# Optimization experiments

Measured on AMD Instinct MI355X. Metric: run time of the kernel, lower is better.

The kernel has to match this reference:

```python
import jax, jax.numpy as jnp
import numpy as np

ATT = 32      # att_size per spatial dim (pooled grid is 32x32, N=1024)
HEADS = 8

def _pool_sum(x, out):
    # adaptive max + adaptive avg pool (exact uniform windows since W%out==0)
    B, C, W, H = x.shape
    kw, kh = W // out, H // out
    r = x.reshape(B, C, out, kw, out, kh)
    return r.max(axis=(3, 5)) + r.mean(axis=(3, 5))

def _lerp_axis(x, out_len, axis):
    in_len = x.shape[axis]
    pos = jnp.arange(out_len, dtype=x.dtype) * ((in_len - 1) / (out_len - 1))
    i0 = jnp.floor(pos).astype(jnp.int32)
    i1 = jnp.minimum(i0 + 1, in_len - 1)
    t = pos - i0.astype(x.dtype)
    shp = [1] * x.ndim
    shp[axis] = out_len
    t = t.reshape(shp)
    return jnp.take(x, i0, axis=axis) * (1 - t) + jnp.take(x, i1, axis=axis) * t

def _upsample_bilinear_ac(x, out_h, out_w):
    # bilinear, align_corners=True (separable)
    return _lerp_axis(_lerp_axis(x, out_h, 2), out_w, 3)

def setup_inputs() -> dict:
    key = jax.random.key(0)
    k1, k2, k3, k4 = jax.random.split(key, 4)
    B, C, W, H = 8, 256, 128, 128
    input1 = jax.random.normal(k1, (B, C, W, H), dtype=jnp.float32)
    input2 = jax.random.normal(k2, (B, C // 2, W, H), dtype=jnp.float32)
    # 1x1 conv: out=C, in=C//2 (kaiming-ish scale)
    conv_w = jax.random.normal(k3, (C, C // 2), dtype=jnp.float32) * (1.0 / np.sqrt(C // 2))
    conv_b = jax.random.normal(k4, (C,), dtype=jnp.float32) * 0.01
    return {"input1": input1, "input2": input2, "conv_w": conv_w, "conv_b": conv_b}

def reference(input1, input2, conv_w, conv_b):
    B, C, W, H = input1.shape
    # channel projection (1x1 conv) since input2 has C//2 channels
    x2 = jnp.einsum('bihw,oi->bohw', input2, conv_w) + conv_b[None, :, None, None]
    p1 = _pool_sum(input1, ATT)   # [B,C,32,32]
    p2 = _pool_sum(x2, ATT)
    N = ATT * ATT
    q = p1.reshape(B, C, N).transpose(2, 0, 1)  # [N,B,C]
    k = p2.reshape(B, C, N).transpose(2, 0, 1)
    v = k
    scale = 1.0 / np.sqrt(C // HEADS)
    w = jnp.einsum('nbc,nec->nbe', q, k)        # [N,B,B]
    w = jax.nn.softmax(w * scale, axis=-1)
    a = jnp.einsum('nbe,nec->nbc', w, v)        # [N,B,C]
    attn = a.transpose(1, 2, 0).reshape(B, C, ATT, ATT)
    up = _upsample_bilinear_ac(attn, W, H)
    return jax.nn.sigmoid(up)
```

## Files before the change

### kernel.cpp

```cpp
#include <hip/hip_runtime.h>
#include <math.h>

namespace {

constexpr int Bn = 8, Cn = 256, CIN = 128, Wd = 128, Hd = 128, ATTn = 32, Nn = ATTn * ATTn;

typedef __attribute__((ext_vector_type(8))) short short8;
typedef __attribute__((ext_vector_type(4))) float f32x4;

__device__ inline unsigned short bf16_rne(float f) {
    unsigned int u = __float_as_uint(f);
    unsigned int r = (u + 0x7FFFu + ((u >> 16) & 1u)) >> 16;
    return (unsigned short)r;
}

__device__ inline int fsw(int px) { return (px ^ (px >> 3)) & 7; }

__global__ __launch_bounds__(512, 4) void front_kernel(const float* __restrict__ in1,
                                                       const float* __restrict__ in2,
                                                       const float* __restrict__ cw,
                                                       const float* __restrict__ cb,
                                                       float* __restrict__ p1t,
                                                       float* __restrict__ p2t) {
    __shared__ __align__(16) unsigned char smem[33792];

    const int t = threadIdx.x;
    const int bid = blockIdx.x;
    const int w = t >> 6;
    const int l = t & 63;

    if (bid < 256) {
        const int b = bid >> 5, oy = bid & 31;
        float* tile = reinterpret_cast<float*>(smem) + w * 1056;
        const int x4 = l & 31, dyp = l >> 5;
        const float* base = in1 + ((size_t)(b * Cn + w * 32) * Wd + oy * 4 + dyp) * Hd + x4 * 4;
#pragma unroll 4
        for (int ch = 0; ch < 32; ++ch) {
            const float* p = base + (size_t)ch * Wd * Hd;
            f32x4 v0 = *reinterpret_cast<const f32x4*>(p);
            f32x4 v1 = *reinterpret_cast<const f32x4*>(p + 2 * Hd);
            float mx = fmaxf(fmaxf(fmaxf(v0[0], v0[1]), fmaxf(v0[2], v0[3])),
                             fmaxf(fmaxf(v1[0], v1[1]), fmaxf(v1[2], v1[3])));
            float sm = ((v0[0] + v0[1]) + (v0[2] + v0[3])) +
                       ((v1[0] + v1[1]) + (v1[2] + v1[3]));
            mx = fmaxf(mx, __shfl_xor(mx, 32));
            sm += __shfl_xor(sm, 32);
            if (l < 32) tile[x4 * 33 + ch] = mx + sm * (1.f / 16.f);
        }
        const int cl = l & 31, oxp = l >> 5;
#pragma unroll
        for (int it = 0; it < 16; ++it) {
            const int ox = it * 2 + oxp;
            const float v = tile[ox * 33 + cl];
            p1t[((size_t)b * Nn + oy * 32 + ox) * Cn + w * 32 + cl] = v;
        }
        return;
    }

    const int bid2 = bid - 256;
    const int b = bid2 >> 7;
    const int r = bid2 & 127;
    const int oy = r >> 2, xq = r & 3;

    f32x4 ra[2][4];
    int x4v[2], rowv[2], k4v[2];
#pragma unroll
    for (int h = 0; h < 2; ++h) {
        const int i = t + h * 512;
        x4v[h] = i & 7; rowv[h] = (i >> 3) & 3; k4v[h] = i >> 5;
        const float* p = in2 + ((size_t)(b * CIN + k4v[h] * 4) * Wd + oy * 4 + rowv[h]) * Hd
                         + xq * 32 + x4v[h] * 4;
#pragma unroll
        for (int kk2 = 0; kk2 < 4; ++kk2)
            ra[h][kk2] = *reinterpret_cast<const f32x4*>(p + (size_t)kk2 * Wd * Hd);
    }

    const int n_lo = l & 15;
    const int khi = l >> 4;
    short8 bfrag[2][4];
#pragma unroll
    for (int f = 0; f < 2; ++f) {
        const int n = w * 32 + f * 16 + n_lo;
#pragma unroll
        for (int kk = 0; kk < 4; ++kk) {
            const float* wp = cw + n * CIN + kk * 32 + khi * 8;
            f32x4 va = *reinterpret_cast<const f32x4*>(wp);
            f32x4 vb = *reinterpret_cast<const f32x4*>(wp + 4);
            short8 s;
            s[0] = (short)bf16_rne(va[0]); s[1] = (short)bf16_rne(va[1]);
            s[2] = (short)bf16_rne(va[2]); s[3] = (short)bf16_rne(va[3]);
            s[4] = (short)bf16_rne(vb[0]); s[5] = (short)bf16_rne(vb[1]);
            s[6] = (short)bf16_rne(vb[2]); s[7] = (short)bf16_rne(vb[3]);
            bfrag[f][kk] = s;
        }
    }
    const float bias2_0 = 2.f * cb[w * 32 + n_lo];
    const float bias2_1 = 2.f * cb[w * 32 + 16 + n_lo];

#pragma unroll
    for (int h = 0; h < 2; ++h) {
#pragma unroll
        for (int j = 0; j < 4; ++j) {
            const int px = x4v[h] * 16 + rowv[h] * 4 + j;
            uint2 u;
            u.x = (unsigned int)bf16_rne(ra[h][0][j]) | ((unsigned int)bf16_rne(ra[h][1][j]) << 16);
            u.y = (unsigned int)bf16_rne(ra[h][2][j]) | ((unsigned int)bf16_rne(ra[h][3][j]) << 16);
            const int off = px * 256 + ((k4v[h] * 8) ^ (fsw(px) << 4));
            *reinterpret_cast<uint2*>(smem + off) = u;
        }
    }
    __syncthreads();

#pragma unroll
    for (int cl = 0; cl < 8; ++cl) {
        f32x4 acc0 = {0.f, 0.f, 0.f, 0.f};
        f32x4 acc1 = {0.f, 0.f, 0.f, 0.f};
        const int px = cl * 16 + n_lo;
        const int sw = fsw(px) << 4;
#pragma unroll
        for (int kk = 0; kk < 4; ++kk) {
            short8 a = *reinterpret_cast<const short8*>(
                smem + px * 256 + ((kk * 64 + khi * 16) ^ sw));
            acc0 = __builtin_amdgcn_mfma_f32_16x16x32_bf16(a, bfrag[0][kk], acc0, 0, 0, 0);
            acc1 = __builtin_amdgcn_mfma_f32_16x16x32_bf16(a, bfrag[1][kk], acc1, 0, 0, 0);
        }
        float mx0 = fmaxf(fmaxf(acc0[0], acc0[1]), fmaxf(acc0[2], acc0[3]));
        float sm0 = (acc0[0] + acc0[1]) + (acc0[2] + acc0[3]);
        float mx1 = fmaxf(fmaxf(acc1[0], acc1[1]), fmaxf(acc1[2], acc1[3]));
        float sm1 = (acc1[0] + acc1[1]) + (acc1[2] + acc1[3]);
        mx0 = fmaxf(mx0, __shfl_xor(mx0, 16)); sm0 += __shfl_xor(sm0, 16);
        mx0 = fmaxf(mx0, __shfl_xor(mx0, 32)); sm0 += __shfl_xor(sm0, 32);
        mx1 = fmaxf(mx1, __shfl_xor(mx1, 16)); sm1 += __shfl_xor(sm1, 16);
        mx1 = fmaxf(mx1, __shfl_xor(mx1, 32)); sm1 += __shfl_xor(sm1, 32);
        if (l < 16) {
            const int cell = oy * 32 + xq * 8 + cl;
            float* dst = p2t + ((size_t)b * Nn + cell) * Cn + w * 32 + n_lo;
            dst[0]  = mx0 + sm0 * (1.f / 16.f) + bias2_0;
            dst[16] = mx1 + sm1 * (1.f / 16.f) + bias2_1;
        }
    }
}

__global__ __launch_bounds__(256) void attn_kernel(const float* __restrict__ p1t,
                                                   const float* __restrict__ p2t,
                                                   float* __restrict__ att) {
    __shared__ float q[Bn][260];
    __shared__ float kk[Bn][260];
    __shared__ float wsm[Bn][8];
    const int n = blockIdx.x, t = threadIdx.x;

#pragma unroll
    for (int i = 0; i < 2; ++i) {
        const int f = t + i * 256;
        const int bb = f >> 6, cq = f & 63;
        const size_t off = ((size_t)bb * Nn + n) * Cn + cq * 4;
        *reinterpret_cast<float4*>(&q[bb][cq * 4])  = *reinterpret_cast<const float4*>(p1t + off);
        *reinterpret_cast<float4*>(&kk[bb][cq * 4]) = *reinterpret_cast<const float4*>(p2t + off);
    }
    __syncthreads();

    {
        const int chunk = t & 3, pair = t >> 2;
        const int e = pair & 7, bb = pair >> 3;
        float s = 0.f;
#pragma unroll
        for (int i = 0; i < 64; ++i)
            s = fmaf(q[bb][i * 4 + chunk], kk[e][i * 4 + chunk], s);
        s += __shfl_xor(s, 1);
        s += __shfl_xor(s, 2);
        s *= 0.17677669529663687f;
        float m = fmaxf(s, __shfl_xor(s, 4));
        m = fmaxf(m, __shfl_xor(m, 8));
        m = fmaxf(m, __shfl_xor(m, 16));
        float p = __expf(s - m);
        float d = p + __shfl_xor(p, 4);
        d += __shfl_xor(d, 8);
        d += __shfl_xor(d, 16);
        if (chunk == 0) wsm[bb][e] = p / d;
    }
    __syncthreads();

    float kv[8];
#pragma unroll
    for (int e = 0; e < 8; ++e) kv[e] = kk[e][t];
#pragma unroll
    for (int bb = 0; bb < 8; ++bb) {
        float s = 0.f;
#pragma unroll
        for (int e = 0; e < 8; ++e) s = fmaf(wsm[bb][e], kv[e], s);
        att[((size_t)bb * Cn + t) * Nn + n] = s;
    }
}

__global__ __launch_bounds__(256) void upsample_kernel(const float* __restrict__ att,
                                                       float* __restrict__ out) {
    __shared__ float tile[ATTn * ATTn];
    int bc = blockIdx.x, t = threadIdx.x;
    reinterpret_cast<float4*>(tile)[t] =
        reinterpret_cast<const float4*>(att + (size_t)bc * Nn)[t];
    __syncthreads();

    int tx = t & 31, ty = t >> 5;
    int xi0[4], xi1[4];
    float xt[4];
#pragma unroll
    for (int j = 0; j < 4; ++j) {
        int x = tx * 4 + j;
        float pos = (float)x * (31.f / 127.f);
        int i0 = (int)pos;
        xi0[j] = i0;
        xi1[j] = min(i0 + 1, 31);
        xt[j] = pos - (float)i0;
    }

    for (int r = 0; r < 16; ++r) {
        int y = ty + r * 8;
        float posy = (float)y * (31.f / 127.f);
        int y0 = (int)posy;
        int y1 = min(y0 + 1, 31);
        float ft = posy - (float)y0;
        float o_[4];
#pragma unroll
        for (int j = 0; j < 4; ++j) {
            float v00 = tile[y0 * 32 + xi0[j]];
            float v01 = tile[y0 * 32 + xi1[j]];
            float v10 = tile[y1 * 32 + xi0[j]];
            float v11 = tile[y1 * 32 + xi1[j]];
            float top = v00 * (1.f - ft) + v10 * ft;
            float bot = v01 * (1.f - ft) + v11 * ft;
            float val = top * (1.f - xt[j]) + bot * xt[j];
            o_[j] = 1.f / (1.f + __expf(-val));
        }
        *reinterpret_cast<float4*>(out + ((size_t)bc * Wd + y) * Hd + tx * 4) =
            make_float4(o_[0], o_[1], o_[2], o_[3]);
    }
}

}

extern "C" void kernel_launch(void* const* d_in, const int* in_sizes, int n_in,
                              void* d_out, int out_size, void* d_ws, size_t ws_size,
                              hipStream_t stream) {
    const float* input1 = (const float*)d_in[0];
    const float* input2 = (const float*)d_in[1];
    const float* conv_w = (const float*)d_in[2];
    const float* conv_b = (const float*)d_in[3];
    float* out = (float*)d_out;

    float* p1t = (float*)d_ws;
    float* p2t = p1t + (size_t)Bn * Cn * Nn;
    float* att = p2t + (size_t)Bn * Cn * Nn;

    front_kernel<<<dim3(1280), dim3(512), 0, stream>>>(input1, input2, conv_w, conv_b, p1t, p2t);
    attn_kernel<<<dim3(Nn), dim3(256), 0, stream>>>(p1t, p2t, att);
    upsample_kernel<<<dim3(Bn * Cn), dim3(256), 0, stream>>>(att, out);
}
```

Before: 110.8 us.

## Split input1 pooling into finer blocks and interleave with conv blocks

The input1 pooling branch is split from 256 large blocks into 2048 smaller blocks, each covering one output row and a 32-channel group. These are interleaved 2:1 with the conv/pool blocks so both kinds of work are spread evenly across CUs. The change also rearranges per-thread loads to 8 contiguous floats, adds shuffle reductions, and uses float2 stores through a shared tile after a barrier. It is meant to fix load imbalance and tail effects from the few heavy pooling blocks, at the cost of more blocks and an extra sync.

```diff
diff --git a/kernel.cpp b/kernel.cpp
--- a/kernel.cpp
+++ b/kernel.cpp
@@ -28,36 +28,49 @@
     const int bid = blockIdx.x;
     const int w = t >> 6;
     const int l = t & 63;
-
-    if (bid < 256) {
-        const int b = bid >> 5, oy = bid & 31;
-        float* tile = reinterpret_cast<float*>(smem) + w * 1056;
-        const int x4 = l & 31, dyp = l >> 5;
-        const float* base = in1 + ((size_t)(b * Cn + w * 32) * Wd + oy * 4 + dyp) * Hd + x4 * 4;
-#pragma unroll 4
-        for (int ch = 0; ch < 32; ++ch) {
-            const float* p = base + (size_t)ch * Wd * Hd;
-            f32x4 v0 = *reinterpret_cast<const f32x4*>(p);
-            f32x4 v1 = *reinterpret_cast<const f32x4*>(p + 2 * Hd);
-            float mx = fmaxf(fmaxf(fmaxf(v0[0], v0[1]), fmaxf(v0[2], v0[3])),
-                             fmaxf(fmaxf(v1[0], v1[1]), fmaxf(v1[2], v1[3])));
-            float sm = ((v0[0] + v0[1]) + (v0[2] + v0[3])) +
-                       ((v1[0] + v1[1]) + (v1[2] + v1[3]));
-            mx = fmaxf(mx, __shfl_xor(mx, 32));
-            sm += __shfl_xor(sm, 32);
-            if (l < 32) tile[x4 * 33 + ch] = mx + sm * (1.f / 16.f);
-        }
-        const int cl = l & 31, oxp = l >> 5;
-#pragma unroll
-        for (int it = 0; it < 16; ++it) {
-            const int ox = it * 2 + oxp;
-            const float v = tile[ox * 33 + cl];
-            p1t[((size_t)b * Nn + oy * 32 + ox) * Cn + w * 32 + cl] = v;
-        }
+    const int g3 = bid / 3;
+    const int r3 = bid - g3 * 3;
+
+    if (r3 != 2) {
+        const int p = g3 * 2 + r3;
+        const int b = p >> 8;
+        const int rem = p & 255;
+        const int oy = rem >> 3, cg = rem & 7;
+        float* tile = reinterpret_cast<float*>(smem);
+
+        const int dy = l >> 4, xp = l & 15;
+        const float* base0 = in1 + (((size_t)(b * Cn + cg * 32 + w * 4) * Wd) + oy * 4 + dy) * Hd
+                             + xp * 8;
+#pragma unroll
+        for (int c4 = 0; c4 < 4; ++c4) {
+            const float* q = base0 + (size_t)c4 * Wd * Hd;
+            f32x4 v0 = *reinterpret_cast<const f32x4*>(q);
+            f32x4 v1 = *reinterpret_cast<const f32x4*>(q + 4);
+            float mx0 = fmaxf(fmaxf(v0[0], v0[1]), fmaxf(v0[2], v0[3]));
+            float sm0 = (v0[0] + v0[1]) + (v0[2] + v0[3]);
+            float mx1 = fmaxf(fmaxf(v1[0], v1[1]), fmaxf(v1[2], v1[3]));
+            float sm1 = (v1[0] + v1[1]) + (v1[2] + v1[3]);
+            mx0 = fmaxf(mx0, __shfl_xor(mx0, 16)); sm0 += __shfl_xor(sm0, 16);
+            mx0 = fmaxf(mx0, __shfl_xor(mx0, 32)); sm0 += __shfl_xor(sm0, 32);
+            mx1 = fmaxf(mx1, __shfl_xor(mx1, 16)); sm1 += __shfl_xor(sm1, 16);
+            mx1 = fmaxf(mx1, __shfl_xor(mx1, 32)); sm1 += __shfl_xor(sm1, 32);
+            if (l < 16) {
+                const int wc = w * 4 + c4;
+                tile[(2 * xp) * 33 + wc]     = mx0 + sm0 * (1.f / 16.f);
+                tile[(2 * xp + 1) * 33 + wc] = mx1 + sm1 * (1.f / 16.f);
+            }
+        }
+        __syncthreads();
+        const int ox = t >> 4, cp = t & 15;
+        float2 o;
+        o.x = tile[ox * 33 + cp * 2];
+        o.y = tile[ox * 33 + cp * 2 + 1];
+        *reinterpret_cast<float2*>(
+            p1t + ((size_t)b * Nn + oy * 32 + ox) * Cn + cg * 32 + cp * 2) = o;
         return;
     }
 
-    const int bid2 = bid - 256;
+    const int bid2 = g3;
     const int b = bid2 >> 7;
     const int r = bid2 & 127;
     const int oy = r >> 2, xq = r & 3;
@@ -251,7 +264,7 @@
     float* p2t = p1t + (size_t)Bn * Cn * Nn;
     float* att = p2t + (size_t)Bn * Cn * Nn;
 
-    front_kernel<<<dim3(1280), dim3(512), 0, stream>>>(input1, input2, conv_w, conv_b, p1t, p2t);
+    front_kernel<<<dim3(3072), dim3(512), 0, stream>>>(input1, input2, conv_w, conv_b, p1t, p2t);
     attn_kernel<<<dim3(Nn), dim3(256), 0, stream>>>(p1t, p2t, att);
     upsample_kernel<<<dim3(Bn * Cn), dim3(256), 0, stream>>>(att, out);
 }
```

New measurement: 112.4 us. About the same (+1.5%).

## Split front kernel into separate pool1 and conv-pool kernels with finer work units

Applied to the files above, without the earlier changes.

The combined front kernel is split in two. One kernel does the max+avg pooling of input1, and the other does the 1x1 conv plus pooling of input2. The new pool1 kernel gives each wave 8 channels of one pooled row instead of 32, uses a small padded LDS tile, and writes the transposed result with 16-byte vector stores. This aims to spread the input1 pooling over many more waves and improve store coalescing, at the cost of an extra kernel launch and losing the overlap between the two heterogeneous block types.

```diff
diff --git a/kernel.cpp b/kernel.cpp
--- a/kernel.cpp
+++ b/kernel.cpp
@@ -16,48 +16,57 @@
 
 __device__ inline int fsw(int px) { return (px ^ (px >> 3)) & 7; }
 
-__global__ __launch_bounds__(512, 4) void front_kernel(const float* __restrict__ in1,
-                                                       const float* __restrict__ in2,
-                                                       const float* __restrict__ cw,
-                                                       const float* __restrict__ cb,
-                                                       float* __restrict__ p1t,
-                                                       float* __restrict__ p2t) {
-    __shared__ __align__(16) unsigned char smem[33792];
+__global__ __launch_bounds__(256, 4) void pool1_kernel(const float* __restrict__ in1,
+                                                       float* __restrict__ p1t) {
+    __shared__ float tile[4][32 * 9];
+    const int t = threadIdx.x, w = t >> 6, l = t & 63;
+    const int gw = blockIdx.x * 4 + w;
+    const int ox = l & 31, half = l >> 5;
+
+#pragma unroll
+    for (int u = 0; u < 2; ++u) {
+        const int unit = gw + u * 4096;
+        const int b = unit >> 10;
+        const int rem = unit & 1023;
+        const int oy = rem >> 5, cg = rem & 31;
+        const float* base = in1 + (((size_t)(b * Cn + cg * 8) * Wd) + oy * 4 + 2 * half) * Hd
+                            + ox * 4;
+        float res[8];
+#pragma unroll
+        for (int c = 0; c < 8; ++c) {
+            const float* p = base + (size_t)c * Wd * Hd;
+            f32x4 a  = *reinterpret_cast<const f32x4*>(p);
+            f32x4 bv = *reinterpret_cast<const f32x4*>(p + Hd);
+            float m = fmaxf(fmaxf(fmaxf(a[0], a[1]), fmaxf(a[2], a[3])),
+                            fmaxf(fmaxf(bv[0], bv[1]), fmaxf(bv[2], bv[3])));
+            float s = ((a[0] + a[1]) + (a[2] + a[3])) + ((bv[0] + bv[1]) + (bv[2] + bv[3]));
+            m = fmaxf(m, __shfl_xor(m, 32));
+            s += __shfl_xor(s, 32);
+            res[c] = m + s * (1.f / 16.f);
+        }
+        if (l < 32) {
+#pragma unroll
+            for (int c = 0; c < 8; ++c) tile[w][ox * 9 + c] = res[c];
+        }
+        const int ox2 = l >> 1, hf = l & 1;
+        f32x4 o;
+#pragma unroll
+        for (int j = 0; j < 4; ++j) o[j] = tile[w][ox2 * 9 + hf * 4 + j];
+        *reinterpret_cast<f32x4*>(
+            p1t + ((size_t)b * Nn + oy * 32 + ox2) * Cn + cg * 8 + hf * 4) = o;
+    }
+}
+
+__global__ __launch_bounds__(512, 4) void convpool_kernel(const float* __restrict__ in2,
+                                                          const float* __restrict__ cw,
+                                                          const float* __restrict__ cb,
+                                                          float* __restrict__ p2t) {
+    __shared__ __align__(16) unsigned char smem[32768];
 
     const int t = threadIdx.x;
-    const int bid = blockIdx.x;
     const int w = t >> 6;
     const int l = t & 63;
-
-    if (bid < 256) {
-        const int b = bid >> 5, oy = bid & 31;
-        float* tile = reinterpret_cast<float*>(smem) + w * 1056;
-        const int x4 = l & 31, dyp = l >> 5;
-        const float* base = in1 + ((size_t)(b * Cn + w * 32) * Wd + oy * 4 + dyp) * Hd + x4 * 4;
-#pragma unroll 4
-        for (int ch = 0; ch < 32; ++ch) {
-            const float* p = base + (size_t)ch * Wd * Hd;
-            f32x4 v0 = *reinterpret_cast<const f32x4*>(p);
-            f32x4 v1 = *reinterpret_cast<const f32x4*>(p + 2 * Hd);
-            float mx = fmaxf(fmaxf(fmaxf(v0[0], v0[1]), fmaxf(v0[2], v0[3])),
-                             fmaxf(fmaxf(v1[0], v1[1]), fmaxf(v1[2], v1[3])));
-            float sm = ((v0[0] + v0[1]) + (v0[2] + v0[3])) +
-                       ((v1[0] + v1[1]) + (v1[2] + v1[3]));
-            mx = fmaxf(mx, __shfl_xor(mx, 32));
-            sm += __shfl_xor(sm, 32);
-            if (l < 32) tile[x4 * 33 + ch] = mx + sm * (1.f / 16.f);
-        }
-        const int cl = l & 31, oxp = l >> 5;
-#pragma unroll
-        for (int it = 0; it < 16; ++it) {
-            const int ox = it * 2 + oxp;
-            const float v = tile[ox * 33 + cl];
-            p1t[((size_t)b * Nn + oy * 32 + ox) * Cn + w * 32 + cl] = v;
-        }
-        return;
-    }
-
-    const int bid2 = bid - 256;
+    const int bid2 = blockIdx.x;
     const int b = bid2 >> 7;
     const int r = bid2 & 127;
     const int oy = r >> 2, xq = r & 3;
@@ -251,7 +260,8 @@
     float* p2t = p1t + (size_t)Bn * Cn * Nn;
     float* att = p2t + (size_t)Bn * Cn * Nn;
 
-    front_kernel<<<dim3(1280), dim3(512), 0, stream>>>(input1, input2, conv_w, conv_b, p1t, p2t);
+    pool1_kernel<<<dim3(1024), dim3(256), 0, stream>>>(input1, p1t);
+    convpool_kernel<<<dim3(1024), dim3(512), 0, stream>>>(input2, conv_w, conv_b, p2t);
     attn_kernel<<<dim3(Nn), dim3(256), 0, stream>>>(p1t, p2t, att);
     upsample_kernel<<<dim3(Bn * Cn), dim3(256), 0, stream>>>(att, out);
 }
```

Result: slower. 114.1 us (+3.0%).

## Split fused pool/conv front kernel into separate pooling and conv-pool kernels

Applied to the files above, without the earlier changes.

The pooling of input1 moves out of the combined front kernel into its own kernel. The new kernel launches 8192 small 256-thread blocks, each handling 8 channels by one output row. The conv+pool part becomes its own kernel with slightly less shared memory. This targets the load imbalance of the old combined grid, where 256 heavy pooling blocks each looped over 32 channels alongside the conv blocks. The cost is an extra kernel launch and the loss of any overlap between the two front phases within one launch.

```diff
diff --git a/kernel.cpp b/kernel.cpp
--- a/kernel.cpp
+++ b/kernel.cpp
@@ -16,48 +16,44 @@
 
 __device__ inline int fsw(int px) { return (px ^ (px >> 3)) & 7; }
 
-__global__ __launch_bounds__(512, 4) void front_kernel(const float* __restrict__ in1,
-                                                       const float* __restrict__ in2,
-                                                       const float* __restrict__ cw,
-                                                       const float* __restrict__ cb,
-                                                       float* __restrict__ p1t,
-                                                       float* __restrict__ p2t) {
-    __shared__ __align__(16) unsigned char smem[33792];
-
+__global__ __launch_bounds__(256) void pool1_kernel(const float* __restrict__ in1,
+                                                    float* __restrict__ p1t) {
+    __shared__ float tile[32 * 9];
     const int t = threadIdx.x;
     const int bid = blockIdx.x;
+    const int cg = bid & 31, oy = (bid >> 5) & 31, b = bid >> 10;
+    const int c = t >> 5, ox = t & 31;
+
+    const float* src = in1 + (((size_t)(b * Cn + cg * 8 + c) * Wd) + oy * 4) * Hd + ox * 4;
+    f32x4 r0 = *reinterpret_cast<const f32x4*>(src);
+    f32x4 r1 = *reinterpret_cast<const f32x4*>(src + Hd);
+    f32x4 r2 = *reinterpret_cast<const f32x4*>(src + 2 * Hd);
+    f32x4 r3 = *reinterpret_cast<const f32x4*>(src + 3 * Hd);
+
+    float mx = fmaxf(fmaxf(fmaxf(r0[0], r0[1]), fmaxf(r0[2], r0[3])),
+                     fmaxf(fmaxf(r1[0], r1[1]), fmaxf(r1[2], r1[3])));
+    mx = fmaxf(mx, fmaxf(fmaxf(fmaxf(r2[0], r2[1]), fmaxf(r2[2], r2[3])),
+                         fmaxf(fmaxf(r3[0], r3[1]), fmaxf(r3[2], r3[3]))));
+    float sm = ((r0[0] + r0[1]) + (r0[2] + r0[3])) + ((r1[0] + r1[1]) + (r1[2] + r1[3]))
+             + ((r2[0] + r2[1]) + (r2[2] + r2[3])) + ((r3[0] + r3[1]) + (r3[2] + r3[3]));
+
+    tile[ox * 9 + c] = mx + sm * (1.f / 16.f);
+    __syncthreads();
+
+    const int ox2 = t >> 3, c2 = t & 7;
+    p1t[((size_t)b * Nn + oy * 32 + ox2) * Cn + cg * 8 + c2] = tile[ox2 * 9 + c2];
+}
+
+__global__ __launch_bounds__(512, 4) void convpool_kernel(const float* __restrict__ in2,
+                                                          const float* __restrict__ cw,
+                                                          const float* __restrict__ cb,
+                                                          float* __restrict__ p2t) {
+    __shared__ __align__(16) unsigned char smem[32768];
+
+    const int t = threadIdx.x;
     const int w = t >> 6;
     const int l = t & 63;
-
-    if (bid < 256) {
-        const int b = bid >> 5, oy = bid & 31;
-        float* tile = reinterpret_cast<float*>(smem) + w * 1056;
-        const int x4 = l & 31, dyp = l >> 5;
-        const float* base = in1 + ((size_t)(b * Cn + w * 32) * Wd + oy * 4 + dyp) * Hd + x4 * 4;
-#pragma unroll 4
-        for (int ch = 0; ch < 32; ++ch) {
-            const float* p = base + (size_t)ch * Wd * Hd;
-            f32x4 v0 = *reinterpret_cast<const f32x4*>(p);
-            f32x4 v1 = *reinterpret_cast<const f32x4*>(p + 2 * Hd);
-            float mx = fmaxf(fmaxf(fmaxf(v0[0], v0[1]), fmaxf(v0[2], v0[3])),
-                             fmaxf(fmaxf(v1[0], v1[1]), fmaxf(v1[2], v1[3])));
-            float sm = ((v0[0] + v0[1]) + (v0[2] + v0[3])) +
-                       ((v1[0] + v1[1]) + (v1[2] + v1[3]));
-            mx = fmaxf(mx, __shfl_xor(mx, 32));
-            sm += __shfl_xor(sm, 32);
-            if (l < 32) tile[x4 * 33 + ch] = mx + sm * (1.f / 16.f);
-        }
-        const int cl = l & 31, oxp = l >> 5;
-#pragma unroll
-        for (int it = 0; it < 16; ++it) {
-            const int ox = it * 2 + oxp;
-            const float v = tile[ox * 33 + cl];
-            p1t[((size_t)b * Nn + oy * 32 + ox) * Cn + w * 32 + cl] = v;
-        }
-        return;
-    }
-
-    const int bid2 = bid - 256;
+    const int bid2 = blockIdx.x;
     const int b = bid2 >> 7;
     const int r = bid2 & 127;
     const int oy = r >> 2, xq = r & 3;
@@ -251,7 +247,8 @@
     float* p2t = p1t + (size_t)Bn * Cn * Nn;
     float* att = p2t + (size_t)Bn * Cn * Nn;
 
-    front_kernel<<<dim3(1280), dim3(512), 0, stream>>>(input1, input2, conv_w, conv_b, p1t, p2t);
+    pool1_kernel<<<dim3(8192), dim3(256), 0, stream>>>(input1, p1t);
+    convpool_kernel<<<dim3(1024), dim3(512), 0, stream>>>(input2, conv_w, conv_b, p2t);
     attn_kernel<<<dim3(Nn), dim3(256), 0, stream>>>(p1t, p2t, att);
     upsample_kernel<<<dim3(Bn * Cn), dim3(256), 0, stream>>>(att, out);
 }
```

Result: no change. 112.3 us (+1.4%).
